# Optimization experiments

Measured on AMD Instinct MI355X. Metric: run time of the kernel, lower is better.

The kernel has to match this reference:

```python
import jax, jax.numpy as jnp
import numpy as np

VOCAB, D, MAX_LEN = 32000, 256, 128
BATCH, SEQ = 32, 128


def setup_inputs() -> dict:
    key = jax.random.key(0)
    ks = jax.random.split(key, 8)
    s = 1.0 / np.sqrt(D)  # torch nn.Linear default init scale
    X = jax.random.randint(ks[0], (BATCH, SEQ), 0, VOCAB)
    emb = jax.random.normal(ks[1], (VOCAB, D), dtype=jnp.float32)
    W_l = jax.random.uniform(ks[2], (D, D), minval=-s, maxval=s, dtype=jnp.float32)
    b_l = jax.random.uniform(ks[3], (D,), minval=-s, maxval=s, dtype=jnp.float32)
    W_r = jax.random.uniform(ks[4], (D, D), minval=-s, maxval=s, dtype=jnp.float32)
    b_r = jax.random.uniform(ks[5], (D,), minval=-s, maxval=s, dtype=jnp.float32)
    W_rn = jax.random.uniform(ks[6], (D, D), minval=-s, maxval=s, dtype=jnp.float32)
    b_rn = jax.random.uniform(ks[7], (D,), minval=-s, maxval=s, dtype=jnp.float32)
    return {"X": X, "emb": emb, "W_l": W_l, "b_l": b_l,
            "W_r": W_r, "b_r": b_r, "W_rn": W_rn, "b_rn": b_rn}


def reference(X, emb, W_l, b_l, W_r, b_r, W_rn, b_rn):
    X = X[:, :MAX_LEN]
    n = X.shape[1]
    Xe = emb[X]                               # (B, n, D) embedding lookup
    Xl = Xe @ W_l.T + b_l                     # (B, n, D)
    Xr = Xe @ W_r.T + b_r                     # (B, n, D)
    # pairwise: pair[b, i, j] = relu(Xl[b, j] + Xr[b, i])  -> (B, n, n, D)
    pair = jax.nn.relu(Xl[:, None, :, :] + Xr[:, :, None, :])
    # linear_rn then sum over (i, j); by linearity: sum(pair) @ W_rn.T + n^2 * b_rn
    pooled = pair.sum(axis=(1, 2))            # (B, D)
    return pooled @ W_rn.T + (n * n) * b_rn   # (B, D)
```

## Files before the change

kernel.cpp:

```cpp
#include <hip/hip_runtime.h>

#define D 256
#define S 128
#define B 32

typedef __attribute__((ext_vector_type(8))) short bf16x8;
typedef __attribute__((ext_vector_type(4))) float f32x4;

__device__ __forceinline__ unsigned short f2bf(float f) {
    union { float f; unsigned u; } v; v.f = f;
    unsigned r = v.u + 0x7FFFu + ((v.u >> 16) & 1u);
    return (unsigned short)(r >> 16);
}
__device__ __forceinline__ float dot4(float4 a, float4 b) {
    return a.x * b.x + a.y * b.y + a.z * b.z + a.w * b.w;
}
__device__ __forceinline__ bf16x8 pack8(const float4 f0, const float4 f1) {
    union { unsigned short u[8]; bf16x8 v; } r;
    r.u[0] = f2bf(f0.x); r.u[1] = f2bf(f0.y); r.u[2] = f2bf(f0.z); r.u[3] = f2bf(f0.w);
    r.u[4] = f2bf(f1.x); r.u[5] = f2bf(f1.y); r.u[6] = f2bf(f1.z); r.u[7] = f2bf(f1.w);
    return r.v;
}

__global__ __launch_bounds__(256) void k12_fused(
    const int* __restrict__ X, const float* __restrict__ emb,
    const float* __restrict__ Wl, const float* __restrict__ Wr,
    const float* __restrict__ bl, const float* __restrict__ br,
    float* __restrict__ pooled)
{
    constexpr int LP = 17;
    __shared__ float lxl[S * LP];
    __shared__ float lxr[S * LP];
    __shared__ float red[256];

    const int b   = blockIdx.x & 31;
    const int dc  = blockIdx.x >> 5;
    const int tid = threadIdx.x;
    const int w   = tid >> 6;
    const int l   = tid & 63;
    const int lm  = l & 15;
    const int lq  = l >> 4;

    const int r0 = w * 32 + lm;
    const int tok0 = X[b * S + r0];
    const int tok1 = X[b * S + r0 + 16];
    const float* a0 = emb + (size_t)tok0 * D;
    const float* a1 = emb + (size_t)tok1 * D;
    const float* bp_l = Wl + (size_t)(dc * 16 + lm) * D + lq * 8;
    const float* bp_r = Wr + (size_t)(dc * 16 + lm) * D + lq * 8;

    f32x4 acc[2][2];
#pragma unroll
    for (int rt = 0; rt < 2; ++rt)
#pragma unroll
        for (int ct = 0; ct < 2; ++ct)
            acc[rt][ct] = (f32x4){0.f, 0.f, 0.f, 0.f};

#pragma unroll
    for (int ks = 0; ks < 8; ++ks) {
        const int k0 = ks * 32 + lq * 8;
        const bf16x8 af0 = pack8(*(const float4*)(a0 + k0),
                                 *(const float4*)(a0 + k0 + 4));
        const bf16x8 af1 = pack8(*(const float4*)(a1 + k0),
                                 *(const float4*)(a1 + k0 + 4));
        const bf16x8 bf_l = pack8(*(const float4*)(bp_l + ks * 32),
                                  *(const float4*)(bp_l + ks * 32 + 4));
        const bf16x8 bf_r = pack8(*(const float4*)(bp_r + ks * 32),
                                  *(const float4*)(bp_r + ks * 32 + 4));
        acc[0][0] = __builtin_amdgcn_mfma_f32_16x16x32_bf16(af0, bf_l, acc[0][0], 0, 0, 0);
        acc[0][1] = __builtin_amdgcn_mfma_f32_16x16x32_bf16(af0, bf_r, acc[0][1], 0, 0, 0);
        acc[1][0] = __builtin_amdgcn_mfma_f32_16x16x32_bf16(af1, bf_l, acc[1][0], 0, 0, 0);
        acc[1][1] = __builtin_amdgcn_mfma_f32_16x16x32_bf16(af1, bf_r, acc[1][1], 0, 0, 0);
    }

    {
        const float bvl = bl[dc * 16 + lm];
        const float bvr = br[dc * 16 + lm];
#pragma unroll
        for (int rt = 0; rt < 2; ++rt) {
#pragma unroll
            for (int i = 0; i < 4; ++i) {
                const int row = w * 32 + rt * 16 + lq * 4 + i;
                lxl[row * LP + lm] = acc[rt][0][i] + bvl;
                lxr[row * LP + lm] = acc[rt][1][i] + bvr;
            }
        }
    }
    __syncthreads();

    const int dl = tid & 15;
    const int ig = tid >> 4;

    float xr[8];
    float sr = 0.f;
#pragma unroll
    for (int u = 0; u < 8; ++u) {
        xr[u] = lxr[(ig * 8 + u) * LP + dl];
        sr += xr[u];
    }

    float sa[8];
#pragma unroll
    for (int u = 0; u < 8; ++u) sa[u] = 0.f;
    float sxl = 0.f;
#pragma unroll 4
    for (int j = 0; j < S; ++j) {
        const float x = lxl[j * LP + dl];
        sxl += x;
#pragma unroll
        for (int u = 0; u < 8; ++u)
            sa[u] += fabsf(x + xr[u]);
    }
    float sabs = ((sa[0] + sa[1]) + (sa[2] + sa[3]))
               + ((sa[4] + sa[5]) + (sa[6] + sa[7]));

    red[tid] = sabs + (float)S * sr;
    __syncthreads();

    if (tid < 16) {
        float tot = 0.f;
#pragma unroll
        for (int g = 0; g < 16; ++g) tot += red[g * 16 + tid];
        pooled[(size_t)b * D + (size_t)dc * 16 + tid] =
            0.5f * ((float)S * sxl + tot);
    }
}

__global__ __launch_bounds__(256) void k3_inplace(
    float* __restrict__ io, const float* __restrict__ Wrn,
    const float* __restrict__ brn)
{
    __shared__ float lp[D];
    const int bb  = blockIdx.x;
    const int tid = threadIdx.x;
    lp[tid] = io[(size_t)bb * D + tid];
    __syncthreads();

    const float4* __restrict__ w4 = (const float4*)(Wrn + (size_t)tid * D);
    const float4* __restrict__ p4 = (const float4*)lp;
    float acc = 0.f;
#pragma unroll 16
    for (int f = 0; f < 64; ++f) acc += dot4(w4[f], p4[f]);

    io[(size_t)bb * D + tid] = acc + (float)(S * S) * brn[tid];
}

extern "C" void kernel_launch(void* const* d_in, const int* in_sizes, int n_in,
                              void* d_out, int out_size, void* d_ws, size_t ws_size,
                              hipStream_t stream) {
    const int*   X   = (const int*)d_in[0];
    const float* emb = (const float*)d_in[1];
    const float* Wl  = (const float*)d_in[2];
    const float* bl  = (const float*)d_in[3];
    const float* Wr  = (const float*)d_in[4];
    const float* br  = (const float*)d_in[5];
    const float* Wrn = (const float*)d_in[6];
    const float* brn = (const float*)d_in[7];
    float* out = (float*)d_out;

    k12_fused<<<B * (D / 16), 256, 0, stream>>>(X, emb, Wl, Wr, bl, br, out);
    k3_inplace<<<B, 256, 0, stream>>>(out, Wrn, brn);
}
```

Baseline: 120.6 us.

## Fuse both kernels into one cooperative launch with grid sync, widen column tile

Merges the pairwise-pooling kernel and the final linear into one cooperative kernel, using grid-wide syncs to pass pooled values through global memory. This removes a second launch and its gap. Each block now covers 32 output columns instead of 16, so the grid drops from 512 to 256 blocks and each block does more MFMA and pairwise work. The cost is lower parallelism, two grid barriers and larger shared-memory tiles.

```diff
diff --git a/kernel.cpp b/kernel.cpp
--- a/kernel.cpp
+++ b/kernel.cpp
@@ -1,4 +1,7 @@
 #include <hip/hip_runtime.h>
+#include <hip/hip_cooperative_groups.h>
+
+namespace cg = cooperative_groups;
 
 #define D 256
 #define S 128
@@ -22,19 +25,23 @@
     return r.v;
 }
 
-__global__ __launch_bounds__(256) void k12_fused(
+__global__ __launch_bounds__(256) void k_all(
     const int* __restrict__ X, const float* __restrict__ emb,
     const float* __restrict__ Wl, const float* __restrict__ Wr,
     const float* __restrict__ bl, const float* __restrict__ br,
-    float* __restrict__ pooled)
+    const float* __restrict__ Wrn, const float* __restrict__ brn,
+    float* __restrict__ out)
 {
-    constexpr int LP = 17;
+    constexpr int LP = 33;
     __shared__ float lxl[S * LP];
     __shared__ float lxr[S * LP];
     __shared__ float red[256];
+    __shared__ float sxl_s[32];
+    __shared__ float lp[D];
 
     const int b   = blockIdx.x & 31;
     const int dc  = blockIdx.x >> 5;
+    const int cl  = dc * 32;
     const int tid = threadIdx.x;
     const int w   = tid >> 6;
     const int l   = tid & 63;
@@ -46,14 +53,16 @@
     const int tok1 = X[b * S + r0 + 16];
     const float* a0 = emb + (size_t)tok0 * D;
     const float* a1 = emb + (size_t)tok1 * D;
-    const float* bp_l = Wl + (size_t)(dc * 16 + lm) * D + lq * 8;
-    const float* bp_r = Wr + (size_t)(dc * 16 + lm) * D + lq * 8;
-
-    f32x4 acc[2][2];
+    const float* bp0 = Wl + (size_t)(cl + lm) * D + lq * 8;
+    const float* bp1 = Wl + (size_t)(cl + 16 + lm) * D + lq * 8;
+    const float* bp2 = Wr + (size_t)(cl + lm) * D + lq * 8;
+    const float* bp3 = Wr + (size_t)(cl + 16 + lm) * D + lq * 8;
+
+    f32x4 acc[2][4];
 #pragma unroll
     for (int rt = 0; rt < 2; ++rt)
 #pragma unroll
-        for (int ct = 0; ct < 2; ++ct)
+        for (int ct = 0; ct < 4; ++ct)
             acc[rt][ct] = (f32x4){0.f, 0.f, 0.f, 0.f};
 
 #pragma unroll
@@ -63,86 +72,112 @@
                                  *(const float4*)(a0 + k0 + 4));
         const bf16x8 af1 = pack8(*(const float4*)(a1 + k0),
                                  *(const float4*)(a1 + k0 + 4));
-        const bf16x8 bf_l = pack8(*(const float4*)(bp_l + ks * 32),
-                                  *(const float4*)(bp_l + ks * 32 + 4));
-        const bf16x8 bf_r = pack8(*(const float4*)(bp_r + ks * 32),
-                                  *(const float4*)(bp_r + ks * 32 + 4));
-        acc[0][0] = __builtin_amdgcn_mfma_f32_16x16x32_bf16(af0, bf_l, acc[0][0], 0, 0, 0);
-        acc[0][1] = __builtin_amdgcn_mfma_f32_16x16x32_bf16(af0, bf_r, acc[0][1], 0, 0, 0);
-        acc[1][0] = __builtin_amdgcn_mfma_f32_16x16x32_bf16(af1, bf_l, acc[1][0], 0, 0, 0);
-        acc[1][1] = __builtin_amdgcn_mfma_f32_16x16x32_bf16(af1, bf_r, acc[1][1], 0, 0, 0);
+        const bf16x8 b0 = pack8(*(const float4*)(bp0 + ks * 32),
+                                *(const float4*)(bp0 + ks * 32 + 4));
+        const bf16x8 b1 = pack8(*(const float4*)(bp1 + ks * 32),
+                                *(const float4*)(bp1 + ks * 32 + 4));
+        const bf16x8 b2 = pack8(*(const float4*)(bp2 + ks * 32),
+                                *(const float4*)(bp2 + ks * 32 + 4));
+        const bf16x8 b3 = pack8(*(const float4*)(bp3 + ks * 32),
+                                *(const float4*)(bp3 + ks * 32 + 4));
+        acc[0][0] = __builtin_amdgcn_mfma_f32_16x16x32_bf16(af0, b0, acc[0][0], 0, 0, 0);
+        acc[1][0] = __builtin_amdgcn_mfma_f32_16x16x32_bf16(af1, b0, acc[1][0], 0, 0, 0);
+        acc[0][1] = __builtin_amdgcn_mfma_f32_16x16x32_bf16(af0, b1, acc[0][1], 0, 0, 0);
+        acc[1][1] = __builtin_amdgcn_mfma_f32_16x16x32_bf16(af1, b1, acc[1][1], 0, 0, 0);
+        acc[0][2] = __builtin_amdgcn_mfma_f32_16x16x32_bf16(af0, b2, acc[0][2], 0, 0, 0);
+        acc[1][2] = __builtin_amdgcn_mfma_f32_16x16x32_bf16(af1, b2, acc[1][2], 0, 0, 0);
+        acc[0][3] = __builtin_amdgcn_mfma_f32_16x16x32_bf16(af0, b3, acc[0][3], 0, 0, 0);
+        acc[1][3] = __builtin_amdgcn_mfma_f32_16x16x32_bf16(af1, b3, acc[1][3], 0, 0, 0);
     }
 
     {
-        const float bvl = bl[dc * 16 + lm];
-        const float bvr = br[dc * 16 + lm];
-#pragma unroll
-        for (int rt = 0; rt < 2; ++rt) {
-#pragma unroll
-            for (int i = 0; i < 4; ++i) {
-                const int row = w * 32 + rt * 16 + lq * 4 + i;
-                lxl[row * LP + lm] = acc[rt][0][i] + bvl;
-                lxr[row * LP + lm] = acc[rt][1][i] + bvr;
+        const float bv[4] = { bl[cl + lm], bl[cl + 16 + lm],
+                              br[cl + lm], br[cl + 16 + lm] };
+#pragma unroll
+        for (int ct = 0; ct < 4; ++ct) {
+            float* dst = (ct < 2) ? lxl : lxr;
+            const int c = (ct & 1) * 16 + lm;
+#pragma unroll
+            for (int rt = 0; rt < 2; ++rt) {
+#pragma unroll
+                for (int i = 0; i < 4; ++i) {
+                    const int row = w * 32 + rt * 16 + lq * 4 + i;
+                    dst[row * LP + c] = acc[rt][ct][i] + bv[ct];
+                }
             }
         }
     }
     __syncthreads();
 
-    const int dl = tid & 15;
-    const int ig = tid >> 4;
-
-    float xr[8];
+    const int dl = tid & 31;
+    const int ig = tid >> 5;
+
+    float xr[16];
     float sr = 0.f;
 #pragma unroll
-    for (int u = 0; u < 8; ++u) {
-        xr[u] = lxr[(ig * 8 + u) * LP + dl];
+    for (int u = 0; u < 16; ++u) {
+        xr[u] = lxr[(ig * 16 + u) * LP + dl];
         sr += xr[u];
     }
 
-    float sa[8];
-#pragma unroll
-    for (int u = 0; u < 8; ++u) sa[u] = 0.f;
+    float sa[16];
+#pragma unroll
+    for (int u = 0; u < 16; ++u) sa[u] = 0.f;
     float sxl = 0.f;
 #pragma unroll 4
     for (int j = 0; j < S; ++j) {
         const float x = lxl[j * LP + dl];
         sxl += x;
 #pragma unroll
-        for (int u = 0; u < 8; ++u)
+        for (int u = 0; u < 16; ++u)
             sa[u] += fabsf(x + xr[u]);
     }
-    float sabs = ((sa[0] + sa[1]) + (sa[2] + sa[3]))
-               + ((sa[4] + sa[5]) + (sa[6] + sa[7]));
+    float sabs = (((sa[0] + sa[1]) + (sa[2] + sa[3]))
+                + ((sa[4] + sa[5]) + (sa[6] + sa[7])))
+               + (((sa[8] + sa[9]) + (sa[10] + sa[11]))
+                + ((sa[12] + sa[13]) + (sa[14] + sa[15])));
 
     red[tid] = sabs + (float)S * sr;
-    __syncthreads();
-
-    if (tid < 16) {
+    if (ig == 0) sxl_s[dl] = sxl;
+    __syncthreads();
+
+    if (tid < 32) {
         float tot = 0.f;
 #pragma unroll
-        for (int g = 0; g < 16; ++g) tot += red[g * 16 + tid];
-        pooled[(size_t)b * D + (size_t)dc * 16 + tid] =
-            0.5f * ((float)S * sxl + tot);
-    }
-}
-
-__global__ __launch_bounds__(256) void k3_inplace(
-    float* __restrict__ io, const float* __restrict__ Wrn,
-    const float* __restrict__ brn)
-{
-    __shared__ float lp[D];
-    const int bb  = blockIdx.x;
-    const int tid = threadIdx.x;
-    lp[tid] = io[(size_t)bb * D + tid];
-    __syncthreads();
-
-    const float4* __restrict__ w4 = (const float4*)(Wrn + (size_t)tid * D);
-    const float4* __restrict__ p4 = (const float4*)lp;
-    float acc = 0.f;
-#pragma unroll 16
-    for (int f = 0; f < 64; ++f) acc += dot4(w4[f], p4[f]);
-
-    io[(size_t)bb * D + tid] = acc + (float)(S * S) * brn[tid];
+        for (int g = 0; g < 8; ++g) tot += red[g * 32 + tid];
+        out[(size_t)b * D + cl + tid] =
+            0.5f * ((float)S * sxl_s[tid] + tot);
+    }
+
+    __threadfence();
+    cg::this_grid().sync();
+
+    lp[tid] = out[(size_t)b * D + tid];
+    __syncthreads();
+
+    const int kg = tid >> 5;
+    const int d  = cl + dl;
+    const float4* __restrict__ w4 = (const float4*)(Wrn + (size_t)d * D) + kg * 8;
+    const float4* __restrict__ p4 = (const float4*)lp + kg * 8;
+    float acc2 = 0.f;
+#pragma unroll
+    for (int f = 0; f < 8; ++f) acc2 += dot4(w4[f], p4[f]);
+
+    red[tid] = acc2;
+    __syncthreads();
+
+    float res = 0.f;
+    if (tid < 32) {
+        float s2 = 0.f;
+#pragma unroll
+        for (int g = 0; g < 8; ++g) s2 += red[g * 32 + tid];
+        res = s2 + (float)(S * S) * brn[cl + tid];
+    }
+
+    __threadfence();
+    cg::this_grid().sync();
+
+    if (tid < 32) out[(size_t)b * D + cl + tid] = res;
 }
 
 extern "C" void kernel_launch(void* const* d_in, const int* in_sizes, int n_in,
@@ -158,6 +193,9 @@
     const float* brn = (const float*)d_in[7];
     float* out = (float*)d_out;
 
-    k12_fused<<<B * (D / 16), 256, 0, stream>>>(X, emb, Wl, Wr, bl, br, out);
-    k3_inplace<<<B, 256, 0, stream>>>(out, Wrn, brn);
-}
+    void* args[] = { (void*)&X, (void*)&emb, (void*)&Wl, (void*)&Wr,
+                     (void*)&bl, (void*)&br, (void*)&Wrn, (void*)&brn,
+                     (void*)&out };
+    hipLaunchCooperativeKernel((const void*)k_all, dim3(B * 8), dim3(256),
+                               args, 0, stream);
+}
```

New measurement: 218.1 us. 1.81x slower.
